# Kernel optimization log

Measured on AMD Instinct MI355X. Metric: run time of the kernel, lower is better.

Reference implementation:

```python
import jax, jax.numpy as jnp
import numpy as np

N_NODES = 100000
N_EDGES = 600000
D_IN = 128
D_HID = 128
D_OUT = 128


def gcn_conv(x, W, b, src, dst, deg_inv_sqrt, num_nodes):
    # PyG GCNConv: h = x @ W, then symmetric-normalized scatter-add over edges
    # (edge list already includes self-loops; deg_inv_sqrt precomputed).
    h = x @ W  # [N, d_out]
    norm = deg_inv_sqrt[src] * deg_inv_sqrt[dst]  # [E+N]
    msgs = h[src] * norm[:, None]  # gather + scale, [E+N, d_out]
    out = jax.ops.segment_sum(msgs, dst, num_segments=num_nodes)
    return out + b


def setup_inputs() -> dict:
    key = jax.random.key(0)
    ks = jax.random.split(key, 8)
    x = jax.random.normal(ks[0], (N_NODES, D_IN), dtype=jnp.float32)
    edge_index = jax.random.randint(ks[1], (2, N_EDGES), 0, N_NODES, dtype=jnp.int32)
    def glorot(k, fan_in, fan_out):
        s = jnp.sqrt(6.0 / (fan_in + fan_out))
        return jax.random.uniform(k, (fan_in, fan_out), jnp.float32, -s, s)
    return {
        "x": x,
        "edge_index": edge_index,
        "W1": glorot(ks[2], D_IN, D_HID), "b1": jnp.zeros((D_HID,), jnp.float32),
        "W2": glorot(ks[3], D_HID, D_HID), "b2": jnp.zeros((D_HID,), jnp.float32),
        "W3": glorot(ks[4], D_HID, D_OUT), "b3": jnp.zeros((D_OUT,), jnp.float32),
    }


def reference(x, edge_index, W1, b1, W2, b2, W3, b3):
    n = x.shape[0]
    loops = jnp.arange(n, dtype=edge_index.dtype)
    src = jnp.concatenate([edge_index[0], loops])  # [E+N]
    dst = jnp.concatenate([edge_index[1], loops])
    # degree over destination nodes (edge weight 1), as in PyG gcn_norm
    deg = jax.ops.segment_sum(jnp.ones_like(dst, dtype=x.dtype), dst, num_segments=n)
    deg_inv_sqrt = jnp.where(deg > 0, jax.lax.rsqrt(jnp.maximum(deg, 1.0)), 0.0)

    h = gcn_conv(x, W1, b1, src, dst, deg_inv_sqrt, n)
    h = jax.nn.relu(h)  # dropout = identity in eval mode
    h = gcn_conv(h, W2, b2, src, dst, deg_inv_sqrt, n)
    h = jax.nn.relu(h)
    out = gcn_conv(h, W3, b3, src, dst, deg_inv_sqrt, n)
    return out
```

## Files before the change

### kernel.cpp

```cpp
#include <hip/hip_runtime.h>

#define D 128
#define SB 256
#define SI 8
#define SCHUNK (SB * SI)

typedef __attribute__((ext_vector_type(8))) short bf16x8;
typedef __attribute__((ext_vector_type(4))) float f32x4;
typedef unsigned int uint32;
typedef unsigned short ushort;

__device__ __forceinline__ ushort bf16rne(float f) {
  uint32 u = __float_as_uint(f);
  uint32 r = u + 0x7FFFu + ((u >> 16) & 1u);
  return (ushort)(r >> 16);
}
__device__ __forceinline__ float bf2f_lo(uint32 h) { return __uint_as_float(h << 16); }
__device__ __forceinline__ float bf2f_hi(uint32 h) { return __uint_as_float(h & 0xFFFF0000u); }
__device__ __forceinline__ uint32 packbf2(float x, float y) {
  return (uint32)bf16rne(x) | ((uint32)bf16rne(y) << 16);
}
__device__ __forceinline__ void acc8(float* a, float w, uint4 h) {
  a[0] += w * bf2f_lo(h.x); a[1] += w * bf2f_hi(h.x);
  a[2] += w * bf2f_lo(h.y); a[3] += w * bf2f_hi(h.y);
  a[4] += w * bf2f_lo(h.z); a[5] += w * bf2f_hi(h.z);
  a[6] += w * bf2f_lo(h.w); a[7] += w * bf2f_hi(h.w);
}


__global__ void prep_kernel(const float* __restrict__ x, ushort* __restrict__ xb, int total4,
                            const int* __restrict__ dst, int* __restrict__ cnt, int E,
                            const float* __restrict__ W1, const float* __restrict__ W2,
                            const float* __restrict__ W3, ushort* __restrict__ Wf,
                            int xbB, int cntB) {
  int b = blockIdx.x;
  int tid = threadIdx.x;
  if (b < xbB) {
    int i = b * 256 + tid;
    if (i < total4) {
      float4 v = ((const float4*)x)[i];
      uint2 o;
      o.x = packbf2(v.x, v.y);
      o.y = packbf2(v.z, v.w);
      ((uint2*)xb)[i] = o;
    }
  } else if (b < xbB + cntB) {
    int e = (b - xbB) * 256 + tid;
    if (e < E) atomicAdd(&cnt[dst[e]], 1);
  } else {
    int idx = (b - xbB - cntB) * 256 + tid;
    int which = idx >> 15;
    int id = idx & 32767;
    const float* W = (which == 0) ? W1 : ((which == 1) ? W2 : W3);
    int j = id & 7;
    int l = (id >> 3) & 63;
    int f = id >> 9;
    int p = f & 1, kc = (f >> 1) & 3, ct = f >> 3;
    int k = kc * 32 + (l >> 4) * 8 + j;
    int col = ct * 16 + (l & 15);
    float w = W[k * D + col];
    ushort hi = bf16rne(w);
    ushort outv = hi;
    if (p) {
      float hf = __uint_as_float((uint32)hi << 16);
      outv = bf16rne(w - hf);
    }
    Wf[idx] = outv;
  }
}


__global__ void scan1_kernel(const int* __restrict__ cnt, int* __restrict__ off,
                             int* __restrict__ bsum, float* __restrict__ dis, int n) {
  __shared__ int tsum[SB];
  int tid = threadIdx.x;
  int base = blockIdx.x * SCHUNK;
  int v[SI];
  int s = 0;
#pragma unroll
  for (int i = 0; i < SI; i++) {
    int idx = base + tid * SI + i;
    v[i] = (idx < n) ? cnt[idx] : 0;
    s += v[i];
  }
  tsum[tid] = s;
  __syncthreads();
  for (int o = 1; o < SB; o <<= 1) {
    int t = (tid >= o) ? tsum[tid - o] : 0;
    __syncthreads();
    tsum[tid] += t;
    __syncthreads();
  }
  int run = tsum[tid] - s;
#pragma unroll
  for (int i = 0; i < SI; i++) {
    int idx = base + tid * SI + i;
    if (idx < n) {
      off[idx] = run;
      dis[idx] = rsqrtf((float)(v[i] + 1));
    }
    run += v[i];
  }
  if (tid == SB - 1) bsum[blockIdx.x] = tsum[tid];
}

__global__ void scan2_kernel(int* bsum, int nb) {
  if (threadIdx.x == 0 && blockIdx.x == 0) {
    int run = 0;
    for (int b = 0; b < nb; b++) { int t = bsum[b]; bsum[b] = run; run += t; }
  }
}

__global__ void scan3_kernel(int* __restrict__ off, const int* __restrict__ bsum,
                             int n, int total) {
  int i = blockIdx.x * blockDim.x + threadIdx.x;
  if (i < n) off[i] += bsum[i / SCHUNK];
  if (i == 0) off[n] = total;
}

__global__ void fill_kernel(const int* __restrict__ src, const int* __restrict__ dst,
                            const int* __restrict__ off, int* __restrict__ cnt,
                            uint2* __restrict__ epack, const float* __restrict__ dis, int E) {
  int e = blockIdx.x * blockDim.x + threadIdx.x;
  if (e >= E) return;
  int s = src[e], d = dst[e];
  int slot = atomicSub(&cnt[d], 1) - 1;
  int p = off[d] + slot;
  uint2 v;
  v.x = (uint32)s;
  v.y = __float_as_uint(dis[s] * dis[d]);
  epack[p] = v;
}


template <int FINAL>
__global__ __launch_bounds__(256, 4) void fused_kernel(const ushort* __restrict__ t,
                                                       const uint2* __restrict__ epack,
                                                       const int* __restrict__ off,
                                                       const float* __restrict__ dis,
                                                       const ushort* __restrict__ Wf,
                                                       const float* __restrict__ bias,
                                                       void* __restrict__ outp, int N) {
  __shared__ char lds[16384];
  int tid = threadIdx.x;
  int row0 = blockIdx.x * 64;
  int lane = tid & 63, wv = tid >> 6;
  int q = lane & 15, g = lane >> 4;
  int qb = q * 16;
  const char* tb = (const char*)t;

#pragma unroll 1
  for (int n4 = 0; n4 < 4; n4++) {
    int r = wv * 16 + n4 * 4 + g;
    int node = row0 + r;
    float a[8];
#pragma unroll
    for (int i = 0; i < 8; i++) a[i] = 0.f;

    if (node < N) {
      uint32 soff = ((uint32)node << 8) + qb;
      uint4 hs = *(const uint4*)(tb + soff);
      int j0 = off[node], j1 = off[node + 1];
      float dsv = dis[node];
      float sw = dsv * dsv;

      auto ldE = [&](int idx) -> uint2 {
        if (idx < j1) return epack[idx];
        uint2 z; z.x = (uint32)node; z.y = 0u; return z;
      };
      int j = j0;
      uint2 e0 = ldE(j), e1 = ldE(j + 1), e2 = ldE(j + 2), e3 = ldE(j + 3);
      while (j < j1) {
        uint4 h0 = *(const uint4*)(tb + ((e0.x << 8) + qb));
        uint4 h1 = *(const uint4*)(tb + ((e1.x << 8) + qb));
        uint4 h2 = *(const uint4*)(tb + ((e2.x << 8) + qb));
        uint4 h3 = *(const uint4*)(tb + ((e3.x << 8) + qb));
        float w0 = __uint_as_float(e0.y), w1 = __uint_as_float(e1.y);
        float w2 = __uint_as_float(e2.y), w3 = __uint_as_float(e3.y);
        int jn = j + 4;
        e0 = ldE(jn); e1 = ldE(jn + 1); e2 = ldE(jn + 2); e3 = ldE(jn + 3);
        acc8(a, w0, h0);
        acc8(a, w1, h1);
        acc8(a, w2, h2);
        acc8(a, w3, h3);
        j = jn;
      }
      acc8(a, sw, hs);
    }
    uint4 pv;
    pv.x = packbf2(a[0], a[1]);
    pv.y = packbf2(a[2], a[3]);
    pv.z = packbf2(a[4], a[5]);
    pv.w = packbf2(a[6], a[7]);
    int boff = (r * 256 + qb) ^ ((r & 7) << 4);
    *(uint4*)(lds + boff) = pv;
  }
  __syncthreads();

  int lr = lane & 15, lg = lane >> 4;
  int m0 = wv * 16;

  bf16x8 af[4];
#pragma unroll
  for (int kc = 0; kc < 4; kc++) {
    int row = m0 + lr;
    int boff = (row * 256 + kc * 64 + lg * 16) ^ ((row & 7) << 4);
    af[kc] = *(bf16x8*)(lds + boff);
  }

  float bcol[8];
#pragma unroll
  for (int ct = 0; ct < 8; ct++) bcol[ct] = bias[ct * 16 + lr];

  f32x4 acc[8];
#pragma unroll
  for (int ct = 0; ct < 8; ct++) acc[ct] = (f32x4){0.f, 0.f, 0.f, 0.f};

#pragma unroll 1
  for (int ct = 0; ct < 8; ct++) {
    bf16x8 bf_[4][2];
#pragma unroll
    for (int kc = 0; kc < 4; kc++)
#pragma unroll
      for (int p = 0; p < 2; p++)
        bf_[kc][p] = *(const bf16x8*)&Wf[(size_t)((((ct * 4 + kc) * 2 + p) * 64 + lane) * 8)];
#pragma unroll
    for (int kc = 0; kc < 4; kc++) {
      acc[ct] = __builtin_amdgcn_mfma_f32_16x16x32_bf16(af[kc], bf_[kc][0], acc[ct], 0, 0, 0);
      acc[ct] = __builtin_amdgcn_mfma_f32_16x16x32_bf16(af[kc], bf_[kc][1], acc[ct], 0, 0, 0);
    }
  }
  __syncthreads();

  if (FINAL) {
    float* out = (float*)outp;
#pragma unroll
    for (int p = 0; p < 2; p++) {
#pragma unroll
      for (int c4 = 0; c4 < 4; c4++) {
        int ct = p * 4 + c4;
#pragma unroll
        for (int r = 0; r < 4; r++) {
          int row = m0 + lg * 4 + r;
          int colb = c4 * 16 + lr;
          float v = acc[ct][r] + bcol[ct];
          int boff = (row * 256 + colb * 4) ^ ((row & 7) << 4);
          *(float*)(lds + boff) = v;
        }
      }
      __syncthreads();
#pragma unroll
      for (int i = 0; i < 4; i++) {
        int f = i * 4096 + tid * 16;
        int row = f >> 8;
        int boff = f ^ ((row & 7) << 4);
        if (row0 + row < N) {
          uint4 v = *(uint4*)(lds + boff);
          *(uint4*)((char*)out + (size_t)(row0 + row) * 512 + p * 256 + (f & 255)) = v;
        }
      }
      if (p == 0) __syncthreads();
    }
  } else {
#pragma unroll
    for (int ct = 0; ct < 8; ct++)
#pragma unroll
      for (int r = 0; r < 4; r++) {
        int row = m0 + lg * 4 + r;
        int col = ct * 16 + lr;
        float v = fmaxf(acc[ct][r] + bcol[ct], 0.f);
        int boff = (row * 256 + col * 2) ^ ((row & 7) << 4);
        *(ushort*)(lds + boff) = bf16rne(v);
      }
    __syncthreads();
    ushort* outb = (ushort*)outp;
#pragma unroll
    for (int i = 0; i < 4; i++) {
      int f = i * 4096 + tid * 16;
      int row = f >> 8;
      int boff = f ^ ((row & 7) << 4);
      if (row0 + row < N) {
        uint4 v = *(uint4*)(lds + boff);
        *(uint4*)((char*)outb + (size_t)(row0 + row) * 256 + (f & 255)) = v;
      }
    }
  }
}


extern "C" void kernel_launch(void* const* d_in, const int* in_sizes, int n_in,
                              void* d_out, int out_size, void* d_ws, size_t ws_size,
                              hipStream_t stream) {
  const float* x  = (const float*)d_in[0];
  const int*   ei = (const int*)d_in[1];
  const float* W1 = (const float*)d_in[2];
  const float* b1 = (const float*)d_in[3];
  const float* W2 = (const float*)d_in[4];
  const float* b2 = (const float*)d_in[5];
  const float* W3 = (const float*)d_in[6];
  const float* b3 = (const float*)d_in[7];
  int N = in_sizes[0] / D;
  int E = in_sizes[1] / 2;
  const int* srcp = ei;
  const int* dstp = ei + E;

  char* wp = (char*)d_ws;
  auto carve = [&](size_t bytes) {
    void* p = (void*)wp;
    wp += (bytes + 255) & ~(size_t)255;
    return p;
  };
  int*    cnt   = (int*)carve((size_t)N * 4);
  int*    off   = (int*)carve((size_t)(N + 1) * 4);
  int*    bsum  = (int*)carve(256 * 4);
  float*  dis   = (float*)carve((size_t)N * 4);
  uint2*  epack = (uint2*)carve((size_t)E * 8);
  ushort* xb    = (ushort*)carve((size_t)N * D * 2);
  ushort* t1    = (ushort*)carve((size_t)N * D * 2);
  ushort* t2    = (ushort*)carve((size_t)N * D * 2);
  ushort* wfall = (ushort*)carve((size_t)3 * 32768 * 2);
  ushort* wf1 = wfall, *wf2 = wfall + 32768, *wf3 = wfall + 65536;

  hipMemsetAsync(cnt, 0, (size_t)N * 4, stream);

  const int tb = 256;
  int total4 = N * D / 4;
  int xbB = (total4 + 255) / 256;
  int cntB = (E + 255) / 256;
  prep_kernel<<<xbB + cntB + 384, 256, 0, stream>>>(x, xb, total4, dstp, cnt, E,
                                                    W1, W2, W3, wfall, xbB, cntB);
  int nb = (N + SCHUNK - 1) / SCHUNK;
  scan1_kernel<<<nb, SB, 0, stream>>>(cnt, off, bsum, dis, N);
  scan2_kernel<<<1, 64, 0, stream>>>(bsum, nb);
  scan3_kernel<<<(N + tb - 1) / tb, tb, 0, stream>>>(off, bsum, N, E);
  fill_kernel<<<(E + tb - 1) / tb, tb, 0, stream>>>(srcp, dstp, off, cnt, epack, dis, E);

  int fb = (N + 63) / 64;
  fused_kernel<0><<<fb, 256, 0, stream>>>(xb, epack, off, dis, wf1, b1, t1, N);
  fused_kernel<0><<<fb, 256, 0, stream>>>(t1, epack, off, dis, wf2, b2, t2, N);
  fused_kernel<1><<<fb, 256, 0, stream>>>(t2, epack, off, dis, wf3, b3, d_out, N);
}
```

Before: 232.7 us.

## Process node pairs per gather loop, replace block barriers with wave-local fences, merge scan passes

The aggregation loop now handles two destination nodes at once, keeping eight neighbor row loads in flight instead of four to hide gather latency. Each wave now reads and writes only its own 16 LDS rows, so block-wide __syncthreads are replaced by a wave-local lgkmcnt wait. The single-thread scan2 kernel is removed: scan3 sums the preceding block totals with a wave shuffle reduction, which saves one launch. The launch-bounds occupancy hint is also dropped. The costs are higher register pressure and idle lanes when the two nodes have very different degrees, and scan3 assumes at most 64 scan chunks.

```diff
diff --git a/kernel.cpp b/kernel.cpp
--- a/kernel.cpp
+++ b/kernel.cpp
@@ -25,6 +25,11 @@
   a[2] += w * bf2f_lo(h.y); a[3] += w * bf2f_hi(h.y);
   a[4] += w * bf2f_lo(h.z); a[5] += w * bf2f_hi(h.z);
   a[6] += w * bf2f_lo(h.w); a[7] += w * bf2f_hi(h.w);
+}
+__device__ __forceinline__ void lds_fence() {
+  __builtin_amdgcn_sched_barrier(0);
+  asm volatile("s_waitcnt lgkmcnt(0)" ::: "memory");
+  __builtin_amdgcn_sched_barrier(0);
 }
 
 
@@ -104,17 +109,21 @@
   if (tid == SB - 1) bsum[blockIdx.x] = tsum[tid];
 }
 
-__global__ void scan2_kernel(int* bsum, int nb) {
-  if (threadIdx.x == 0 && blockIdx.x == 0) {
-    int run = 0;
-    for (int b = 0; b < nb; b++) { int t = bsum[b]; bsum[b] = run; run += t; }
-  }
-}
-
 __global__ void scan3_kernel(int* __restrict__ off, const int* __restrict__ bsum,
                              int n, int total) {
-  int i = blockIdx.x * blockDim.x + threadIdx.x;
-  if (i < n) off[i] += bsum[i / SCHUNK];
+  __shared__ int cbase;
+  int b = blockIdx.x;
+  int tid = threadIdx.x;
+  int c = (b * 256) / SCHUNK;
+  if (tid < 64) {
+    int v = (tid < c) ? bsum[tid] : 0;
+#pragma unroll
+    for (int o = 32; o; o >>= 1) v += __shfl_down(v, o);
+    if (tid == 0) cbase = v;
+  }
+  __syncthreads();
+  int i = b * 256 + tid;
+  if (i < n) off[i] += cbase;
   if (i == 0) off[n] = total;
 }
 
@@ -134,13 +143,13 @@
 
 
 template <int FINAL>
-__global__ __launch_bounds__(256, 4) void fused_kernel(const ushort* __restrict__ t,
-                                                       const uint2* __restrict__ epack,
-                                                       const int* __restrict__ off,
-                                                       const float* __restrict__ dis,
-                                                       const ushort* __restrict__ Wf,
-                                                       const float* __restrict__ bias,
-                                                       void* __restrict__ outp, int N) {
+__global__ __launch_bounds__(256) void fused_kernel(const ushort* __restrict__ t,
+                                                    const uint2* __restrict__ epack,
+                                                    const int* __restrict__ off,
+                                                    const float* __restrict__ dis,
+                                                    const ushort* __restrict__ Wf,
+                                                    const float* __restrict__ bias,
+                                                    void* __restrict__ outp, int N) {
   __shared__ char lds[16384];
   int tid = threadIdx.x;
   int row0 = blockIdx.x * 64;
@@ -150,52 +159,69 @@
   const char* tb = (const char*)t;
 
 #pragma unroll 1
-  for (int n4 = 0; n4 < 4; n4++) {
-    int r = wv * 16 + n4 * 4 + g;
-    int node = row0 + r;
-    float a[8];
-#pragma unroll
-    for (int i = 0; i < 8; i++) a[i] = 0.f;
-
-    if (node < N) {
-      uint32 soff = ((uint32)node << 8) + qb;
-      uint4 hs = *(const uint4*)(tb + soff);
-      int j0 = off[node], j1 = off[node + 1];
-      float dsv = dis[node];
-      float sw = dsv * dsv;
-
-      auto ldE = [&](int idx) -> uint2 {
-        if (idx < j1) return epack[idx];
-        uint2 z; z.x = (uint32)node; z.y = 0u; return z;
-      };
-      int j = j0;
-      uint2 e0 = ldE(j), e1 = ldE(j + 1), e2 = ldE(j + 2), e3 = ldE(j + 3);
-      while (j < j1) {
-        uint4 h0 = *(const uint4*)(tb + ((e0.x << 8) + qb));
-        uint4 h1 = *(const uint4*)(tb + ((e1.x << 8) + qb));
-        uint4 h2 = *(const uint4*)(tb + ((e2.x << 8) + qb));
-        uint4 h3 = *(const uint4*)(tb + ((e3.x << 8) + qb));
-        float w0 = __uint_as_float(e0.y), w1 = __uint_as_float(e1.y);
-        float w2 = __uint_as_float(e2.y), w3 = __uint_as_float(e3.y);
-        int jn = j + 4;
-        e0 = ldE(jn); e1 = ldE(jn + 1); e2 = ldE(jn + 2); e3 = ldE(jn + 3);
-        acc8(a, w0, h0);
-        acc8(a, w1, h1);
-        acc8(a, w2, h2);
-        acc8(a, w3, h3);
-        j = jn;
-      }
-      acc8(a, sw, hs);
-    }
-    uint4 pv;
-    pv.x = packbf2(a[0], a[1]);
-    pv.y = packbf2(a[2], a[3]);
-    pv.z = packbf2(a[4], a[5]);
-    pv.w = packbf2(a[6], a[7]);
-    int boff = (r * 256 + qb) ^ ((r & 7) << 4);
-    *(uint4*)(lds + boff) = pv;
-  }
-  __syncthreads();
+  for (int pair = 0; pair < 2; pair++) {
+    int rA = wv * 16 + pair * 8 + g;
+    int rB = rA + 4;
+    int nodeA = row0 + rA, nodeB = row0 + rB;
+    bool vA = nodeA < N, vB = nodeB < N;
+    int nA = vA ? nodeA : 0, nB = vB ? nodeB : 0;
+
+    float aA[8], aB[8];
+#pragma unroll
+    for (int i = 0; i < 8; i++) { aA[i] = 0.f; aB[i] = 0.f; }
+
+    uint4 hsA = *(const uint4*)(tb + (((uint32)nA << 8) + qb));
+    uint4 hsB = *(const uint4*)(tb + (((uint32)nB << 8) + qb));
+    int j0A = vA ? off[nodeA] : 0, j1A = vA ? off[nodeA + 1] : 0;
+    int j0B = vB ? off[nodeB] : 0, j1B = vB ? off[nodeB + 1] : 0;
+    float dA = vA ? dis[nodeA] : 0.f, dB = vB ? dis[nodeB] : 0.f;
+    float swA = dA * dA, swB = dB * dB;
+
+    auto ldA = [&](int idx) -> uint2 {
+      if (idx < j1A) return epack[idx];
+      uint2 z; z.x = (uint32)nA; z.y = 0u; return z;
+    };
+    auto ldB = [&](int idx) -> uint2 {
+      if (idx < j1B) return epack[idx];
+      uint2 z; z.x = (uint32)nB; z.y = 0u; return z;
+    };
+
+    int jA = j0A, jB = j0B;
+    uint2 eA0 = ldA(jA), eA1 = ldA(jA + 1), eA2 = ldA(jA + 2), eA3 = ldA(jA + 3);
+    uint2 eB0 = ldB(jB), eB1 = ldB(jB + 1), eB2 = ldB(jB + 2), eB3 = ldB(jB + 3);
+    while (jA < j1A || jB < j1B) {
+      uint4 hA0 = *(const uint4*)(tb + ((eA0.x << 8) + qb));
+      uint4 hA1 = *(const uint4*)(tb + ((eA1.x << 8) + qb));
+      uint4 hA2 = *(const uint4*)(tb + ((eA2.x << 8) + qb));
+      uint4 hA3 = *(const uint4*)(tb + ((eA3.x << 8) + qb));
+      uint4 hB0 = *(const uint4*)(tb + ((eB0.x << 8) + qb));
+      uint4 hB1 = *(const uint4*)(tb + ((eB1.x << 8) + qb));
+      uint4 hB2 = *(const uint4*)(tb + ((eB2.x << 8) + qb));
+      uint4 hB3 = *(const uint4*)(tb + ((eB3.x << 8) + qb));
+      float wA0 = __uint_as_float(eA0.y), wA1 = __uint_as_float(eA1.y);
+      float wA2 = __uint_as_float(eA2.y), wA3 = __uint_as_float(eA3.y);
+      float wB0 = __uint_as_float(eB0.y), wB1 = __uint_as_float(eB1.y);
+      float wB2 = __uint_as_float(eB2.y), wB3 = __uint_as_float(eB3.y);
+      jA += 4; jB += 4;
+      eA0 = ldA(jA); eA1 = ldA(jA + 1); eA2 = ldA(jA + 2); eA3 = ldA(jA + 3);
+      eB0 = ldB(jB); eB1 = ldB(jB + 1); eB2 = ldB(jB + 2); eB3 = ldB(jB + 3);
+      acc8(aA, wA0, hA0); acc8(aA, wA1, hA1); acc8(aA, wA2, hA2); acc8(aA, wA3, hA3);
+      acc8(aB, wB0, hB0); acc8(aB, wB1, hB1); acc8(aB, wB2, hB2); acc8(aB, wB3, hB3);
+    }
+    acc8(aA, swA, hsA);
+    acc8(aB, swB, hsB);
+
+    uint4 pA, pB;
+    pA.x = packbf2(aA[0], aA[1]); pA.y = packbf2(aA[2], aA[3]);
+    pA.z = packbf2(aA[4], aA[5]); pA.w = packbf2(aA[6], aA[7]);
+    pB.x = packbf2(aB[0], aB[1]); pB.y = packbf2(aB[2], aB[3]);
+    pB.z = packbf2(aB[4], aB[5]); pB.w = packbf2(aB[6], aB[7]);
+    int boffA = (rA * 256 + qb) ^ ((rA & 7) << 4);
+    int boffB = (rB * 256 + qb) ^ ((rB & 7) << 4);
+    *(uint4*)(lds + boffA) = pA;
+    *(uint4*)(lds + boffB) = pB;
+  }
+  lds_fence();
 
   int lr = lane & 15, lg = lane >> 4;
   int m0 = wv * 16;
@@ -230,7 +256,7 @@
       acc[ct] = __builtin_amdgcn_mfma_f32_16x16x32_bf16(af[kc], bf_[kc][1], acc[ct], 0, 0, 0);
     }
   }
-  __syncthreads();
+  lds_fence();
 
   if (FINAL) {
     float* out = (float*)outp;
@@ -248,10 +274,10 @@
           *(float*)(lds + boff) = v;
         }
       }
-      __syncthreads();
+      lds_fence();
 #pragma unroll
       for (int i = 0; i < 4; i++) {
-        int f = i * 4096 + tid * 16;
+        int f = wv * 4096 + i * 1024 + lane * 16;
         int row = f >> 8;
         int boff = f ^ ((row & 7) << 4);
         if (row0 + row < N) {
@@ -259,7 +285,7 @@
           *(uint4*)((char*)out + (size_t)(row0 + row) * 512 + p * 256 + (f & 255)) = v;
         }
       }
-      if (p == 0) __syncthreads();
+      lds_fence();
     }
   } else {
 #pragma unroll
@@ -272,11 +298,11 @@
         int boff = (row * 256 + col * 2) ^ ((row & 7) << 4);
         *(ushort*)(lds + boff) = bf16rne(v);
       }
-    __syncthreads();
+    lds_fence();
     ushort* outb = (ushort*)outp;
 #pragma unroll
     for (int i = 0; i < 4; i++) {
-      int f = i * 4096 + tid * 16;
+      int f = wv * 4096 + i * 1024 + lane * 16;
       int row = f >> 8;
       int boff = f ^ ((row & 7) << 4);
       if (row0 + row < N) {
@@ -331,7 +357,6 @@
                                                     W1, W2, W3, wfall, xbB, cntB);
   int nb = (N + SCHUNK - 1) / SCHUNK;
   scan1_kernel<<<nb, SB, 0, stream>>>(cnt, off, bsum, dis, N);
-  scan2_kernel<<<1, 64, 0, stream>>>(bsum, nb);
   scan3_kernel<<<(N + tb - 1) / tb, tb, 0, stream>>>(off, bsum, N, E);
   fill_kernel<<<(E + tb - 1) / tb, tb, 0, stream>>>(srcp, dstp, off, cnt, epack, dis, E);
 
```

After: 251.6 us. +8.1%, slower.
